# Performance work log

Hardware: AMD Instinct MI355X
Metric: run time of the kernel (lower is better)

Reference implementation:

```python
import jax, jax.numpy as jnp
import numpy as np

HID, HEADS, HD = 512, 8, 64  # hid_dim, n_heads, head_dim
NEG = -1e10


def setup_inputs() -> dict:
    key = jax.random.key(0)
    ks = jax.random.split(key, 12)
    B, S = 4, 2048
    inp = {
        'query': jax.random.normal(ks[0], (B, S, HID), jnp.float32),
        'key': jax.random.normal(ks[1], (B, S, HID), jnp.float32),
        'value': jax.random.normal(ks[2], (B, S, HID), jnp.float32),
        'mask': jnp.ones((B, 1, 1, S), jnp.int32),
    }
    sc = 1.0 / np.sqrt(HID)
    for i, n in enumerate(['Wq', 'Wk', 'Wv', 'Wo']):
        inp[n] = jax.random.uniform(ks[3 + i], (HID, HID), jnp.float32, -sc, sc)
    for i, n in enumerate(['bq', 'bk', 'bv', 'bo']):
        inp[n] = jax.random.uniform(ks[7 + i], (HID,), jnp.float32, -sc, sc)
    return inp


def reference(query, key, value, mask, Wq, Wk, Wv, Wo, bq, bk, bv, bo):
    B = query.shape[0]

    def proj(x, W, b):
        # torch Linear: x @ W.T + b; then split heads -> [B, H, S, HD]
        y = jnp.einsum('bsd,ed->bse', x, W) + b
        return y.reshape(B, -1, HEADS, HD).transpose(0, 2, 1, 3)

    Q = proj(query, Wq, bq)
    K = proj(key, Wk, bk)
    V = proj(value, Wv, bv)
    scale = jnp.sqrt(jnp.float32(HD))
    E = jnp.einsum('bhqd,bhkd->bhqk', Q, K) / scale  # [B,H,Sq,Sk]
    E = jnp.where(mask == 0, NEG, E)
    A = jax.nn.softmax(E, axis=-1)  # dropout p=0 -> identity
    out = jnp.einsum('bhqk,bhkd->bhqd', A, V)
    out = out.transpose(0, 2, 1, 3).reshape(B, -1, HID)
    return jnp.einsum('bsd,ed->bse', out, Wo) + bo
```

## Files before the change

### kernel.cpp

```cpp
#include <hip/hip_runtime.h>
#include <hip/hip_bf16.h>


typedef __bf16 v8bf __attribute__((ext_vector_type(8)));
typedef __bf16 v4bf __attribute__((ext_vector_type(4)));
typedef float  v4f  __attribute__((ext_vector_type(4)));
typedef short  v4s  __attribute__((ext_vector_type(4)));

#define MFMA16(a, b, c) __builtin_amdgcn_mfma_f32_16x16x32_bf16((a), (b), (c), 0, 0, 0)

__device__ inline v4f MFMA_PV(v4bf a, v4bf b, v4f c) {
    return __builtin_amdgcn_mfma_f32_16x16x16bf16_1k(
        __builtin_bit_cast(v4s, a), __builtin_bit_cast(v4s, b), c, 0, 0, 0);
}

#define QSCALE 0.1803368801111f

__device__ inline v8bf cvt8(const float* __restrict__ p) {
    const v4f f0 = *(const v4f*)p;
    const v4f f1 = *(const v4f*)(p + 4);
    v8bf r;
    r[0] = (__bf16)f0[0]; r[1] = (__bf16)f0[1]; r[2] = (__bf16)f0[2]; r[3] = (__bf16)f0[3];
    r[4] = (__bf16)f1[0]; r[5] = (__bf16)f1[1]; r[6] = (__bf16)f1[2]; r[7] = (__bf16)f1[3];
    return r;
}

__global__ __launch_bounds__(256) void cvt_w(
    const float* __restrict__ Wq, const float* __restrict__ Wk,
    const float* __restrict__ Wv, const float* __restrict__ Wo,
    __bf16* __restrict__ out)
{
    const int idx = (blockIdx.x * 256 + threadIdx.x) * 4;
    const int w = idx >> 18, off = idx & 262143;
    const float* src = (w == 0) ? Wq : (w == 1) ? Wk : (w == 2) ? Wv : Wo;
    const float sc = (w == 0) ? QSCALE : 1.0f;
    const v4f x = *(const v4f*)(src + off);
    v4bf y;
    y[0] = (__bf16)(x[0] * sc); y[1] = (__bf16)(x[1] * sc);
    y[2] = (__bf16)(x[2] * sc); y[3] = (__bf16)(x[3] * sc);
    *(v4bf*)(out + idx) = y;
}

__global__ __launch_bounds__(256) void qkv_gemm(
    const float* __restrict__ xq, const float* __restrict__ xk, const float* __restrict__ xv,
    const __bf16* __restrict__ Wb,
    const float* __restrict__ bq, const float* __restrict__ bk, const float* __restrict__ bv,
    __bf16* __restrict__ Qo, __bf16* __restrict__ Ko, __bf16* __restrict__ VTo)
{
    const int z = blockIdx.z;
    const float*  x    = (z == 0) ? xq : (z == 1) ? xk : xv;
    const __bf16* W    = Wb + (size_t)z * 262144;
    const float*  bias = (z == 0) ? bq : (z == 1) ? bk : bv;
    const float   bsc  = (z == 0) ? QSCALE : 1.0f;

    const int tid = threadIdx.x, wave = tid >> 6, lane = tid & 63;
    const int quad = lane >> 4, r = lane & 15;
    const int wm = wave >> 1, wn = wave & 1;
    const int row0 = blockIdx.x * 128, col0 = blockIdx.y * 128;

    __shared__ __align__(16) __bf16 As[8192];
    __shared__ __align__(16) __bf16 Bs[8192];

    const float*  aptr[4];
    const __bf16* bptr[4];
    int adst[4], bdst[4];
    for (int j = 0; j < 4; j++) {
        const int e = tid + 256 * j;
        const int seg = e >> 6, ln = e & 63;
        aptr[j] = x + (size_t)(row0 + (seg >> 1) * 16 + (ln & 15)) * 512
                    + (seg & 1) * 32 + (ln >> 4) * 8;
        adst[j] = e * 8;
        const int segb = wave * 4 + j;
        bptr[j] = W + (size_t)(col0 + (segb >> 1) * 16 + r) * 512
                    + (segb & 1) * 32 + quad * 8;
        bdst[j] = (segb * 64 + lane) * 8;
    }

    v4f acc[4][4] = {};
    v8bf aReg[4], bReg[4];
    for (int j = 0; j < 4; j++) {
        aReg[j] = cvt8(aptr[j]);
        bReg[j] = *(const v8bf*)bptr[j];
    }

    for (int ki = 0; ki < 8; ki++) {
        __syncthreads();
        for (int j = 0; j < 4; j++) {
            *(v8bf*)&As[adst[j]] = aReg[j];
            *(v8bf*)&Bs[bdst[j]] = bReg[j];
        }
        __syncthreads();
        if (ki < 7) {
            const int kk = (ki + 1) * 64;
            for (int j = 0; j < 4; j++) {
                aReg[j] = cvt8(aptr[j] + kk);
                bReg[j] = *(const v8bf*)(bptr[j] + kk);
            }
        }
        for (int kc = 0; kc < 2; kc++) {
            v8bf a[4], b[4];
            for (int i = 0; i < 4; i++)
                a[i] = ((const v8bf*)As)[((wm * 4 + i) * 2 + kc) * 64 + lane];
            for (int i = 0; i < 4; i++)
                b[i] = ((const v8bf*)Bs)[((wn * 4 + i) * 2 + kc) * 64 + lane];
            for (int mi = 0; mi < 4; mi++)
                for (int ni = 0; ni < 4; ni++)
                    acc[mi][ni] = MFMA16(a[mi], b[ni], acc[mi][ni]);
        }
    }

    for (int ni = 0; ni < 4; ni++) {
        const int n = col0 + wn * 64 + ni * 16 + r;
        const float bv_ = bias[n] * bsc;
        const int hh = n >> 6, hd = n & 63;
        for (int mi = 0; mi < 4; mi++) {
            const int mbase = row0 + wm * 64 + mi * 16 + quad * 4;
            const int bb = mbase >> 11, s0 = mbase & 2047;
            if (z == 2) {
                v4bf pk;
                for (int i = 0; i < 4; i++)
                    pk[i] = (__bf16)(acc[mi][ni][i] + bv_);
                *(v4bf*)&VTo[((size_t)((bb * 8 + hh) * 64 + hd)) * 2048 + s0] = pk;
            } else {
                __bf16* dst = (z == 0) ? Qo : Ko;
                for (int i = 0; i < 4; i++)
                    dst[((size_t)((bb * 8 + hh) * 2048 + s0 + i)) * 64 + hd] =
                        (__bf16)(acc[mi][ni][i] + bv_);
            }
        }
    }
}

__global__ __launch_bounds__(256) void attn(
    const __bf16* __restrict__ Q, const __bf16* __restrict__ K,
    const __bf16* __restrict__ VT, const int* __restrict__ mask,
    __bf16* __restrict__ AO)
{
    const int bh = blockIdx.y, b = bh >> 3, h = bh & 7;
    const int tid = threadIdx.x, wave = tid >> 6, lane = tid & 63;
    const int quad = lane >> 4, r = lane & 15;
    const int q0 = blockIdx.x * 64 + wave * 16;

    const __bf16* Qb = Q  + (size_t)bh * 2048 * 64;
    const __bf16* Kb = K  + (size_t)bh * 2048 * 64;
    const __bf16* Vb = VT + (size_t)bh * 64 * 2048;
    const int*    mb = mask + (size_t)b * 2048;

    __shared__ __align__(16) __bf16 Kls[4096];
    __shared__ __align__(16) __bf16 Vls[64 * 72];
    __shared__ float biasF[2048];

    for (int i = tid; i < 2048; i += 256)
        biasF[i] = (mb[i] != 0) ? 0.f : -1e10f;

    const int e1 = tid, e2 = tid + 256;
    int seg, l_, t_, h_, rr, qd;
    seg = e1 >> 6; l_ = e1 & 63; t_ = seg >> 1; h_ = seg & 1; rr = l_ & 15; qd = l_ >> 4;
    const __bf16* kg1 = Kb + (size_t)(16 * t_ + rr) * 64 + h_ * 32 + qd * 8;
    seg = e2 >> 6; l_ = e2 & 63; t_ = seg >> 1; h_ = seg & 1; rr = l_ & 15; qd = l_ >> 4;
    const __bf16* kg2 = Kb + (size_t)(16 * t_ + rr) * 64 + h_ * 32 + qd * 8;

    const int hd1 = tid >> 3, c1 = tid & 7;
    const __bf16* vg1 = Vb + (size_t)hd1 * 2048 + c1 * 8;
    const __bf16* vg2 = Vb + (size_t)(hd1 + 32) * 2048 + c1 * 8;
    const int dV1 = hd1 * 72 + c1 * 8, dV2 = (hd1 + 32) * 72 + c1 * 8;

    v8bf qf0 = *(const v8bf*)(Qb + (size_t)(q0 + r) * 64 +      quad * 8);
    v8bf qf1 = *(const v8bf*)(Qb + (size_t)(q0 + r) * 64 + 32 + quad * 8);

    float ssum = 0.f;
    v4f o[4] = {};

    v8bf ks1 = *(const v8bf*)kg1, ks2 = *(const v8bf*)kg2;
    v8bf vs1 = *(const v8bf*)vg1, vs2 = *(const v8bf*)vg2;

    const int vbase = r * 72 + quad * 4;

    for (int t = 0; t < 32; t++) {
        __syncthreads();
        ((v8bf*)Kls)[e1] = ks1; ((v8bf*)Kls)[e2] = ks2;
        *(v8bf*)&Vls[dV1] = vs1; *(v8bf*)&Vls[dV2] = vs2;
        __syncthreads();
        if (t < 31) {
            const int k0n = (t + 1) * 64;
            ks1 = *(const v8bf*)(kg1 + (size_t)k0n * 64);
            ks2 = *(const v8bf*)(kg2 + (size_t)k0n * 64);
            vs1 = *(const v8bf*)(vg1 + k0n);
            vs2 = *(const v8bf*)(vg2 + k0n);
        }
        const int k0 = t * 64;

        v4f sa[4];
        for (int tt = 0; tt < 4; tt++) {
            const v4f bias4 = *(const v4f*)&biasF[k0 + tt * 16 + quad * 4];
            v8bf kf0 = ((const v8bf*)Kls)[(tt * 2 + 0) * 64 + lane];
            v8bf kf1 = ((const v8bf*)Kls)[(tt * 2 + 1) * 64 + lane];
            sa[tt] = MFMA16(kf0, qf0, bias4);
            sa[tt] = MFMA16(kf1, qf1, sa[tt]);
        }

        v4bf pf[4];
        for (int tt = 0; tt < 4; tt++) {
            for (int i = 0; i < 4; i++) {
                const float p = exp2f(sa[tt][i]);
                ssum += p;
                pf[tt][i] = (__bf16)p;
            }
        }

        for (int g = 0; g < 4; g++)
            for (int t2 = 0; t2 < 4; t2++) {
                const v4bf vf = *(const v4bf*)&Vls[t2 * 1152 + vbase + g * 16];
                o[t2] = MFMA_PV(vf, pf[g], o[t2]);
            }
    }

    ssum += __shfl_xor(ssum, 16);
    ssum += __shfl_xor(ssum, 32);
    const float inv = 1.0f / ssum;

    __bf16* dst = AO + ((size_t)b * 2048 + q0 + r) * 512 + h * 64 + quad * 4;
    for (int t2 = 0; t2 < 4; t2++) {
        v4bf pk;
        for (int i = 0; i < 4; i++)
            pk[i] = (__bf16)(o[t2][i] * inv);
        *(v4bf*)(dst + t2 * 16) = pk;
    }
}

__global__ __launch_bounds__(256) void out_gemm(
    const __bf16* __restrict__ Ai, const __bf16* __restrict__ W,
    const float* __restrict__ bias, float* __restrict__ y)
{
    const int tid = threadIdx.x, wave = tid >> 6, lane = tid & 63;
    const int quad = lane >> 4, r = lane & 15;
    const int wm = wave >> 1, wn = wave & 1;
    const int row0 = blockIdx.x * 128, col0 = blockIdx.y * 128;

    __shared__ __align__(16) __bf16 As[8192];
    __shared__ __align__(16) __bf16 Bs[8192];

    const __bf16* aptr[4];
    const __bf16* bptr[4];
    int dst_[4];
    for (int j = 0; j < 4; j++) {
        const int segb = wave * 4 + j;
        aptr[j] = Ai + (size_t)(row0 + (segb >> 1) * 16 + r) * 512 + (segb & 1) * 32 + quad * 8;
        bptr[j] = W  + (size_t)(col0 + (segb >> 1) * 16 + r) * 512 + (segb & 1) * 32 + quad * 8;
        dst_[j] = (segb * 64 + lane) * 8;
    }

    v4f acc[4][4] = {};
    v8bf aReg[4], bReg[4];
    for (int j = 0; j < 4; j++) {
        aReg[j] = *(const v8bf*)aptr[j];
        bReg[j] = *(const v8bf*)bptr[j];
    }

    for (int ki = 0; ki < 8; ki++) {
        __syncthreads();
        for (int j = 0; j < 4; j++) {
            *(v8bf*)&As[dst_[j]] = aReg[j];
            *(v8bf*)&Bs[dst_[j]] = bReg[j];
        }
        __syncthreads();
        if (ki < 7) {
            const int kk = (ki + 1) * 64;
            for (int j = 0; j < 4; j++) {
                aReg[j] = *(const v8bf*)(aptr[j] + kk);
                bReg[j] = *(const v8bf*)(bptr[j] + kk);
            }
        }
        for (int kc = 0; kc < 2; kc++) {
            v8bf a[4], b[4];
            for (int i = 0; i < 4; i++)
                a[i] = ((const v8bf*)As)[((wm * 4 + i) * 2 + kc) * 64 + lane];
            for (int i = 0; i < 4; i++)
                b[i] = ((const v8bf*)Bs)[((wn * 4 + i) * 2 + kc) * 64 + lane];
            for (int mi = 0; mi < 4; mi++)
                for (int ni = 0; ni < 4; ni++)
                    acc[mi][ni] = MFMA16(a[mi], b[ni], acc[mi][ni]);
        }
    }

    for (int ni = 0; ni < 4; ni++) {
        const int n = col0 + wn * 64 + ni * 16 + r;
        const float bv_ = bias[n];
        for (int mi = 0; mi < 4; mi++) {
            const int mbase = row0 + wm * 64 + mi * 16 + quad * 4;
            for (int i = 0; i < 4; i++)
                y[(size_t)(mbase + i) * 512 + n] = acc[mi][ni][i] + bv_;
        }
    }
}

extern "C" void kernel_launch(void* const* d_in, const int* in_sizes, int n_in,
                              void* d_out, int out_size, void* d_ws, size_t ws_size,
                              hipStream_t stream)
{
    const float* q    = (const float*)d_in[0];
    const float* k    = (const float*)d_in[1];
    const float* v    = (const float*)d_in[2];
    const int*   mask = (const int*)d_in[3];
    const float* Wq   = (const float*)d_in[4];
    const float* Wk   = (const float*)d_in[5];
    const float* Wv   = (const float*)d_in[6];
    const float* Wo   = (const float*)d_in[7];
    const float* bq   = (const float*)d_in[8];
    const float* bk   = (const float*)d_in[9];
    const float* bv   = (const float*)d_in[10];
    const float* bo   = (const float*)d_in[11];

    __bf16* ws  = (__bf16*)d_ws;
    __bf16* Qw  = ws;
    __bf16* Kw  = ws + 4194304;
    __bf16* VTw = ws + 8388608;
    __bf16* AOw = ws + 12582912;
    __bf16* Wb  = ws + 16777216;

    cvt_w<<<dim3(1024), 256, 0, stream>>>(Wq, Wk, Wv, Wo, Wb);
    qkv_gemm<<<dim3(64, 4, 3), 256, 0, stream>>>(q, k, v, Wb, bq, bk, bv, Qw, Kw, VTw);
    attn<<<dim3(32, 32), 256, 0, stream>>>(Qw, Kw, VTw, mask, AOw);
    out_gemm<<<dim3(64, 4), 256, 0, stream>>>(AOw, Wb + 786432, bo, (float*)d_out);
}
```

Baseline: 239.9 us.

## Process two query tiles per wave in attention and pre-swizzle V in LDS

```diff
diff --git a/kernel.cpp b/kernel.cpp
--- a/kernel.cpp
+++ b/kernel.cpp
@@ -139,7 +139,7 @@
     const int bh = blockIdx.y, b = bh >> 3, h = bh & 7;
     const int tid = threadIdx.x, wave = tid >> 6, lane = tid & 63;
     const int quad = lane >> 4, r = lane & 15;
-    const int q0 = blockIdx.x * 64 + wave * 16;
+    const int q0 = blockIdx.x * 128 + wave * 32;
 
     const __bf16* Qb = Q  + (size_t)bh * 2048 * 64;
     const __bf16* Kb = K  + (size_t)bh * 2048 * 64;
@@ -147,84 +147,91 @@
     const int*    mb = mask + (size_t)b * 2048;
 
     __shared__ __align__(16) __bf16 Kls[4096];
-    __shared__ __align__(16) __bf16 Vls[64 * 72];
+    __shared__ __align__(16) __bf16 Vls[4096];
     __shared__ float biasF[2048];
 
     for (int i = tid; i < 2048; i += 256)
         biasF[i] = (mb[i] != 0) ? 0.f : -1e10f;
 
     const int e1 = tid, e2 = tid + 256;
-    int seg, l_, t_, h_, rr, qd;
-    seg = e1 >> 6; l_ = e1 & 63; t_ = seg >> 1; h_ = seg & 1; rr = l_ & 15; qd = l_ >> 4;
-    const __bf16* kg1 = Kb + (size_t)(16 * t_ + rr) * 64 + h_ * 32 + qd * 8;
-    seg = e2 >> 6; l_ = e2 & 63; t_ = seg >> 1; h_ = seg & 1; rr = l_ & 15; qd = l_ >> 4;
-    const __bf16* kg2 = Kb + (size_t)(16 * t_ + rr) * 64 + h_ * 32 + qd * 8;
-
-    const int hd1 = tid >> 3, c1 = tid & 7;
-    const __bf16* vg1 = Vb + (size_t)hd1 * 2048 + c1 * 8;
-    const __bf16* vg2 = Vb + (size_t)(hd1 + 32) * 2048 + c1 * 8;
-    const int dV1 = hd1 * 72 + c1 * 8, dV2 = (hd1 + 32) * 72 + c1 * 8;
-
-    v8bf qf0 = *(const v8bf*)(Qb + (size_t)(q0 + r) * 64 +      quad * 8);
-    v8bf qf1 = *(const v8bf*)(Qb + (size_t)(q0 + r) * 64 + 32 + quad * 8);
-
-    float ssum = 0.f;
-    v4f o[4] = {};
+    int seg, l_, t_, h_;
+    seg = e1 >> 6; l_ = e1 & 63; t_ = seg >> 1; h_ = seg & 1;
+    const __bf16* kg1 = Kb + (size_t)(16 * t_ + (l_ & 15)) * 64 + h_ * 32 + (l_ >> 4) * 8;
+    seg = e2 >> 6; l_ = e2 & 63; t_ = seg >> 1; h_ = seg & 1;
+    const __bf16* kg2 = Kb + (size_t)(16 * t_ + (l_ & 15)) * 64 + h_ * 32 + (l_ >> 4) * 8;
+
+    const __bf16* vgp[4];
+    int ve[4];
+    for (int j = 0; j < 4; j++) {
+        const int e = tid + 256 * j;
+        const int s = e >> 6, l = e & 63;
+        vgp[j] = Vb + (size_t)((s >> 2) * 16 + (l & 15)) * 2048 + (s & 3) * 16 + (l >> 4) * 4;
+        ve[j] = e;
+    }
+
+    v8bf qf[2][2];
+    for (int qg = 0; qg < 2; qg++) {
+        const __bf16* qp = Qb + (size_t)(q0 + qg * 16 + r) * 64;
+        qf[qg][0] = *(const v8bf*)(qp +      quad * 8);
+        qf[qg][1] = *(const v8bf*)(qp + 32 + quad * 8);
+    }
+
+    float ssum[2] = {0.f, 0.f};
+    v4f o[2][4] = {};
 
     v8bf ks1 = *(const v8bf*)kg1, ks2 = *(const v8bf*)kg2;
-    v8bf vs1 = *(const v8bf*)vg1, vs2 = *(const v8bf*)vg2;
-
-    const int vbase = r * 72 + quad * 4;
+    v4bf vs[4];
+    for (int j = 0; j < 4; j++) vs[j] = *(const v4bf*)vgp[j];
 
     for (int t = 0; t < 32; t++) {
         __syncthreads();
         ((v8bf*)Kls)[e1] = ks1; ((v8bf*)Kls)[e2] = ks2;
-        *(v8bf*)&Vls[dV1] = vs1; *(v8bf*)&Vls[dV2] = vs2;
+        for (int j = 0; j < 4; j++) ((v4bf*)Vls)[ve[j]] = vs[j];
         __syncthreads();
         if (t < 31) {
             const int k0n = (t + 1) * 64;
             ks1 = *(const v8bf*)(kg1 + (size_t)k0n * 64);
             ks2 = *(const v8bf*)(kg2 + (size_t)k0n * 64);
-            vs1 = *(const v8bf*)(vg1 + k0n);
-            vs2 = *(const v8bf*)(vg2 + k0n);
+            for (int j = 0; j < 4; j++) vs[j] = *(const v4bf*)(vgp[j] + k0n);
         }
         const int k0 = t * 64;
 
-        v4f sa[4];
+        v4bf pf[2][4];
         for (int tt = 0; tt < 4; tt++) {
             const v4f bias4 = *(const v4f*)&biasF[k0 + tt * 16 + quad * 4];
             v8bf kf0 = ((const v8bf*)Kls)[(tt * 2 + 0) * 64 + lane];
             v8bf kf1 = ((const v8bf*)Kls)[(tt * 2 + 1) * 64 + lane];
-            sa[tt] = MFMA16(kf0, qf0, bias4);
-            sa[tt] = MFMA16(kf1, qf1, sa[tt]);
-        }
-
-        v4bf pf[4];
-        for (int tt = 0; tt < 4; tt++) {
-            for (int i = 0; i < 4; i++) {
-                const float p = exp2f(sa[tt][i]);
-                ssum += p;
-                pf[tt][i] = (__bf16)p;
+            for (int qg = 0; qg < 2; qg++) {
+                v4f sa = MFMA16(kf0, qf[qg][0], bias4);
+                sa = MFMA16(kf1, qf[qg][1], sa);
+                for (int i = 0; i < 4; i++) {
+                    const float p = exp2f(sa[i]);
+                    ssum[qg] += p;
+                    pf[qg][tt][i] = (__bf16)p;
+                }
             }
         }
 
         for (int g = 0; g < 4; g++)
             for (int t2 = 0; t2 < 4; t2++) {
-                const v4bf vf = *(const v4bf*)&Vls[t2 * 1152 + vbase + g * 16];
-                o[t2] = MFMA_PV(vf, pf[g], o[t2]);
-            }
-    }
-
-    ssum += __shfl_xor(ssum, 16);
-    ssum += __shfl_xor(ssum, 32);
-    const float inv = 1.0f / ssum;
-
-    __bf16* dst = AO + ((size_t)b * 2048 + q0 + r) * 512 + h * 64 + quad * 4;
-    for (int t2 = 0; t2 < 4; t2++) {
-        v4bf pk;
-        for (int i = 0; i < 4; i++)
-            pk[i] = (__bf16)(o[t2][i] * inv);
-        *(v4bf*)(dst + t2 * 16) = pk;
+                const v4bf vf = ((const v4bf*)Vls)[(t2 * 4 + g) * 64 + lane];
+                o[0][t2] = MFMA_PV(vf, pf[0][g], o[0][t2]);
+                o[1][t2] = MFMA_PV(vf, pf[1][g], o[1][t2]);
+            }
+    }
+
+    for (int qg = 0; qg < 2; qg++) {
+        float s = ssum[qg];
+        s += __shfl_xor(s, 16);
+        s += __shfl_xor(s, 32);
+        const float inv = 1.0f / s;
+        __bf16* dst = AO + ((size_t)b * 2048 + q0 + qg * 16 + r) * 512 + h * 64 + quad * 4;
+        for (int t2 = 0; t2 < 4; t2++) {
+            v4bf pk;
+            for (int i = 0; i < 4; i++)
+                pk[i] = (__bf16)(o[qg][t2][i] * inv);
+            *(v4bf*)(dst + t2 * 16) = pk;
+        }
     }
 }
 
@@ -320,6 +327,6 @@
 
     cvt_w<<<dim3(1024), 256, 0, stream>>>(Wq, Wk, Wv, Wo, Wb);
     qkv_gemm<<<dim3(64, 4, 3), 256, 0, stream>>>(q, k, v, Wb, bq, bk, bv, Qw, Kw, VTw);
-    attn<<<dim3(32, 32), 256, 0, stream>>>(Qw, Kw, VTw, mask, AOw);
+    attn<<<dim3(16, 32), 256, 0, stream>>>(Qw, Kw, VTw, mask, AOw);
     out_gemm<<<dim3(64, 4), 256, 0, stream>>>(AOw, Wb + 786432, bo, (float*)d_out);
 }
```

New measurement: 241.4 us. About the same (+0.6%).
